# Optimization experiments

Measured on AMD Instinct MI355X. Metric: run time of the kernel, lower is better.

Reference implementation:

```python
import jax, jax.numpy as jnp
import numpy as np


def binarize_weight(w, scale=True):
    # Per-output-row mean-abs scale (dim=1 of [out, in]) times sign.
    # sign(0) -> 0 matches torch.sign semantics.
    s = jnp.mean(jnp.abs(w), axis=1, keepdims=True) if scale else jnp.ones((w.shape[0], 1), w.dtype)
    return jnp.sign(w) * s


def setup_inputs() -> dict:
    key = jax.random.key(0)
    kx, kw = jax.random.split(key)
    B, S, D_IN, D_OUT = 4, 2048, 4096, 4096
    x = jax.random.normal(kx, (B, S, D_IN), dtype=jnp.float32)
    # kaiming_normal_ with nonlinearity='linear': std = 1/sqrt(fan_in)
    weight = jax.random.normal(kw, (D_OUT, D_IN), dtype=jnp.float32) * (1.0 / np.sqrt(D_IN))
    return {"x": x, "weight": weight}


def reference(x, weight):
    w_b = binarize_weight(weight, scale=True)  # [out, in]
    # F.linear(x, w_b): x @ w_b.T
    return jnp.einsum("bsi,oi->bso", x, w_b)
```

## Files before the change

kernel.cpp:

```cpp
#include <hip/hip_runtime.h>
#include <hip/hip_bf16.h>
#include <stdint.h>

typedef int  iv4   __attribute__((ext_vector_type(4)));
typedef float f32x4 __attribute__((ext_vector_type(4)));

#define K_DIM 4096
#define N_DIM 4096

__global__ __launch_bounds__(256) void convert_x_i8(const float* __restrict__ x,
                                                    char* __restrict__ xq,
                                                    float* __restrict__ sx) {
    const int row = blockIdx.x;
    const int tid = threadIdx.x;
    const float* xr = x + (long long)row * K_DIM + tid * 16;

    float4 v0 = *(const float4*)(xr + 0);
    float4 v1 = *(const float4*)(xr + 4);
    float4 v2 = *(const float4*)(xr + 8);
    float4 v3 = *(const float4*)(xr + 12);

    float m = fabsf(v0.x);
    m = fmaxf(m, fabsf(v0.y)); m = fmaxf(m, fabsf(v0.z)); m = fmaxf(m, fabsf(v0.w));
    m = fmaxf(m, fabsf(v1.x)); m = fmaxf(m, fabsf(v1.y)); m = fmaxf(m, fabsf(v1.z)); m = fmaxf(m, fabsf(v1.w));
    m = fmaxf(m, fabsf(v2.x)); m = fmaxf(m, fabsf(v2.y)); m = fmaxf(m, fabsf(v2.z)); m = fmaxf(m, fabsf(v2.w));
    m = fmaxf(m, fabsf(v3.x)); m = fmaxf(m, fabsf(v3.y)); m = fmaxf(m, fabsf(v3.z)); m = fmaxf(m, fabsf(v3.w));

    #pragma unroll
    for (int d = 32; d > 0; d >>= 1) m = fmaxf(m, __shfl_xor(m, d));
    __shared__ float red[4];
    const int lane = tid & 63, wid = tid >> 6;
    if (lane == 0) red[wid] = m;
    __syncthreads();
    float rmax = fmaxf(fmaxf(red[0], red[1]), fmaxf(red[2], red[3]));
    rmax = fmaxf(rmax, 1e-20f);
    if (tid == 0) sx[row] = rmax * (1.0f / 127.0f);

    const float q = 127.0f / rmax;
    union { char c[16]; int4 v; } u;
    const float vals[16] = {v0.x, v0.y, v0.z, v0.w, v1.x, v1.y, v1.z, v1.w,
                            v2.x, v2.y, v2.z, v2.w, v3.x, v3.y, v3.z, v3.w};
    #pragma unroll
    for (int i = 0; i < 16; ++i) u.c[i] = (char)__float2int_rn(vals[i] * q);
    *(int4*)(xq + (long long)row * K_DIM + tid * 16) = u.v;
}

__global__ __launch_bounds__(256) void convert_w_i8(const float* __restrict__ w,
                                                    char* __restrict__ wq,
                                                    float* __restrict__ sw) {
    const int row = blockIdx.x;
    const int tid = threadIdx.x;
    const float* wr = w + (long long)row * K_DIM + tid * 16;

    float sum = 0.f;
    union { char c[16]; int4 v; } u;
    #pragma unroll
    for (int j = 0; j < 4; ++j) {
        float4 v = *(const float4*)(wr + j * 4);
        sum += fabsf(v.x) + fabsf(v.y) + fabsf(v.z) + fabsf(v.w);
        u.c[j * 4 + 0] = (char)((v.x > 0.f) - (v.x < 0.f));
        u.c[j * 4 + 1] = (char)((v.y > 0.f) - (v.y < 0.f));
        u.c[j * 4 + 2] = (char)((v.z > 0.f) - (v.z < 0.f));
        u.c[j * 4 + 3] = (char)((v.w > 0.f) - (v.w < 0.f));
    }
    *(int4*)(wq + (long long)row * K_DIM + tid * 16) = u.v;

    #pragma unroll
    for (int d = 32; d > 0; d >>= 1) sum += __shfl_down(sum, d);
    __shared__ float red[4];
    const int lane = tid & 63, wid = tid >> 6;
    if (lane == 0) red[wid] = sum;
    __syncthreads();
    if (tid == 0) sw[row] = (red[0] + red[1] + red[2] + red[3]) * (1.0f / (float)K_DIM);
}

struct SOp { const char* g; int row0; int kt; char* l; };

__device__ __forceinline__ void stage_half(const SOp s, int wid, int lane) {
    const int r      = s.row0 + wid * 16 + (lane >> 2);
    const int srcoff = s.kt + ((((lane & 3) ^ ((lane >> 3) & 3))) << 4);
    const char* src  = s.g + (long long)r * K_DIM + srcoff;
    __builtin_amdgcn_global_load_lds(
        (const __attribute__((address_space(1))) void*)src,
        (__attribute__((address_space(3))) void*)(s.l + wid * 1024), 16, 0, 0);
}

__device__ __forceinline__ iv4 ldsr(const char* t, int row, int c) {
    const int off = row * 64 + ((c ^ ((row >> 1) & 3)) << 4);
    return *(const iv4*)(t + off);
}

__device__ __forceinline__ void read_a0(iv4 (&a)[4], const char* tA, int wm, int l15, int c) {
    #pragma unroll
    for (int mi = 0; mi < 4; ++mi) a[mi] = ldsr(tA, wm * 128 + mi * 16 + l15, c);
}
__device__ __forceinline__ void read_a1(iv4 (&a)[4], const char* tA, int wm, int l15, int c) {
    #pragma unroll
    for (int mi = 0; mi < 4; ++mi) a[mi] = ldsr(tA, wm * 128 + 64 + mi * 16 + l15, c);
}
__device__ __forceinline__ void read_b0(iv4 (&b)[2], const char* tB, int wn, int l15, int c) {
    #pragma unroll
    for (int ni = 0; ni < 2; ++ni) b[ni] = ldsr(tB, wn * 64 + ni * 16 + l15, c);
}
__device__ __forceinline__ void read_b1(iv4 (&b)[2], const char* tB, int wn, int l15, int c) {
    #pragma unroll
    for (int ni = 0; ni < 2; ++ni) b[ni] = ldsr(tB, wn * 64 + 32 + ni * 16 + l15, c);
}

template<bool S0, bool S1, bool S2, bool S3, int WN>
__device__ __forceinline__ void kgroup(const char* __restrict__ tA,
                                       const char* __restrict__ tB,
                                       SOp s0, SOp s1, SOp s2, SOp s3,
                                       iv4 (&acc)[8][4],
                                       int wm, int wn, int wid, int lane)
{
    const int l15 = lane & 15;
    const int c   = lane >> 4;
    iv4 a0[4], a1[4], b0[2], b1[2];

    read_a0(a0, tA, wm, l15, c);
    read_b0(b0, tB, wn, l15, c);
    if constexpr (S0) stage_half(s0, wid, lane);
    __builtin_amdgcn_s_barrier();
    __builtin_amdgcn_s_setprio(1);
    #pragma unroll
    for (int mi = 0; mi < 4; ++mi)
        #pragma unroll
        for (int ni = 0; ni < 2; ++ni)
            acc[mi][ni] = __builtin_amdgcn_mfma_i32_16x16x64_i8(
                a0[mi], b0[ni], acc[mi][ni], 0, 0, 0);
    __builtin_amdgcn_s_setprio(0);
    __builtin_amdgcn_s_barrier();

    read_b1(b1, tB, wn, l15, c);
    if constexpr (S1) stage_half(s1, wid, lane);
    __builtin_amdgcn_s_barrier();
    __builtin_amdgcn_s_setprio(1);
    #pragma unroll
    for (int mi = 0; mi < 4; ++mi)
        #pragma unroll
        for (int ni = 0; ni < 2; ++ni)
            acc[mi][2 + ni] = __builtin_amdgcn_mfma_i32_16x16x64_i8(
                a0[mi], b1[ni], acc[mi][2 + ni], 0, 0, 0);
    __builtin_amdgcn_s_setprio(0);
    __builtin_amdgcn_s_barrier();

    read_a1(a1, tA, wm, l15, c);
    if constexpr (S2) stage_half(s2, wid, lane);
    __builtin_amdgcn_s_barrier();
    __builtin_amdgcn_s_setprio(1);
    #pragma unroll
    for (int mi = 0; mi < 4; ++mi)
        #pragma unroll
        for (int ni = 0; ni < 2; ++ni)
            acc[4 + mi][ni] = __builtin_amdgcn_mfma_i32_16x16x64_i8(
                a1[mi], b0[ni], acc[4 + mi][ni], 0, 0, 0);
    __builtin_amdgcn_s_setprio(0);
    __builtin_amdgcn_s_barrier();

    if constexpr (S3) stage_half(s3, wid, lane);
    __builtin_amdgcn_s_barrier();
    __builtin_amdgcn_s_setprio(1);
    #pragma unroll
    for (int mi = 0; mi < 4; ++mi)
        #pragma unroll
        for (int ni = 0; ni < 2; ++ni)
            acc[4 + mi][2 + ni] = __builtin_amdgcn_mfma_i32_16x16x64_i8(
                a1[mi], b1[ni], acc[4 + mi][2 + ni], 0, 0, 0);
    __builtin_amdgcn_s_setprio(0);
    if constexpr (WN == 1)      asm volatile("s_waitcnt vmcnt(1)" ::: "memory");
    else if constexpr (WN == 0) asm volatile("s_waitcnt vmcnt(0)" ::: "memory");
    if constexpr (WN >= 0) __builtin_amdgcn_s_barrier();
}

__global__ __launch_bounds__(512, 2) void bitlinear_gemm_i8(
    const char* __restrict__ A, const char* __restrict__ B,
    const float* __restrict__ sx, const float* __restrict__ sw,
    float* __restrict__ C, int M)
{
    extern __shared__ char smem[];
    char* As0 = smem;
    char* As1 = smem + 16384;
    char* Bs0 = smem + 32768;
    char* Bs1 = smem + 49152;

    const int tid = threadIdx.x, lane = tid & 63, wid = tid >> 6;
    const int wm = wid >> 2, wn = wid & 3;

    const int nbid = (int)blockIdx.x;
    const int cpx  = (int)gridDim.x >> 3;
    const int swz  = (nbid & 7) * cpx + (nbid >> 3);
    const int ntn  = N_DIM / 256;
    const int tm = swz / ntn, tn = swz % ntn;

    const char* gA = A + (long long)tm * 256 * K_DIM;
    const char* gB = B + (long long)tn * 256 * K_DIM;

    iv4 acc[8][4];
    #pragma unroll
    for (int i = 0; i < 8; ++i)
        #pragma unroll
        for (int j = 0; j < 4; ++j) acc[i][j] = (iv4){0, 0, 0, 0};

    stage_half({gA,   0,  0, As0},        wid, lane);
    stage_half({gA, 128,  0, As0 + 8192}, wid, lane);
    stage_half({gB,   0,  0, Bs0},        wid, lane);
    stage_half({gB, 128,  0, Bs0 + 8192}, wid, lane);
    stage_half({gA,   0, 64, As1},        wid, lane);
    asm volatile("s_waitcnt vmcnt(1)" ::: "memory");
    __builtin_amdgcn_s_barrier();

    kgroup<true, true, true, true, 1>(As0, Bs0,
        {gA, 128,  64, As1 + 8192}, {gB, 0,  64, Bs1},
        {gB, 128,  64, Bs1 + 8192}, {gA, 0, 128, As0},
        acc, wm, wn, wid, lane);
    #pragma unroll 1
    for (int i = 0; i < 30; ++i) {
        const int kt = (2 * i + 1) * 64;
        kgroup<true, true, true, true, 1>(As1, Bs1,
            {gA, 128, kt + 64,  As0 + 8192}, {gB, 0, kt + 64,  Bs0},
            {gB, 128, kt + 64,  Bs0 + 8192}, {gA, 0, kt + 128, As1},
            acc, wm, wn, wid, lane);
        kgroup<true, true, true, true, 1>(As0, Bs0,
            {gA, 128, kt + 128, As1 + 8192}, {gB, 0, kt + 128, Bs1},
            {gB, 128, kt + 128, Bs1 + 8192}, {gA, 0, kt + 192, As0},
            acc, wm, wn, wid, lane);
    }
    kgroup<true, true, true, true, 1>(As1, Bs1,
        {gA, 128, 62 * 64, As0 + 8192}, {gB, 0, 62 * 64, Bs0},
        {gB, 128, 62 * 64, Bs0 + 8192}, {gA, 0, 63 * 64, As1},
        acc, wm, wn, wid, lane);
    kgroup<true, true, true, false, 0>(As0, Bs0,
        {gA, 128, 63 * 64, As1 + 8192}, {gB, 0, 63 * 64, Bs1},
        {gB, 128, 63 * 64, Bs1 + 8192}, {gA, 0, 0, As0},
        acc, wm, wn, wid, lane);
    kgroup<false, false, false, false, -1>(As1, Bs1,
        {gA, 0, 0, As0}, {gA, 0, 0, As0}, {gA, 0, 0, As0}, {gA, 0, 0, As0},
        acc, wm, wn, wid, lane);

    const long long m0 = (long long)tm * 256 + wm * 128;
    const long long n0 = (long long)tn * 256 + wn * 64;
    float swv[4];
    #pragma unroll
    for (int ni = 0; ni < 4; ++ni) swv[ni] = sw[n0 + ni * 16 + (lane & 15)];
    #pragma unroll
    for (int mi = 0; mi < 8; ++mi) {
        const long long rowb = m0 + mi * 16 + (lane >> 4) * 4;
        float sxr[4];
        #pragma unroll
        for (int j = 0; j < 4; ++j) sxr[j] = sx[rowb + j];
        #pragma unroll
        for (int ni = 0; ni < 4; ++ni) {
            const long long col = n0 + ni * 16 + (lane & 15);
            #pragma unroll
            for (int j = 0; j < 4; ++j)
                C[(rowb + j) * N_DIM + col] = (float)acc[mi][ni][j] * swv[ni] * sxr[j];
        }
    }
}

__global__ void bitlinear_naive_kernel(const float* __restrict__ x,
                                       const float* __restrict__ w,
                                       float* __restrict__ out, long long total) {
    const long long idx = (long long)blockIdx.x * blockDim.x + threadIdx.x;
    if (idx >= total) return;
    const long long m = idx / N_DIM;
    const long long o = idx % N_DIM;
    const float* xr = x + m * K_DIM;
    const float* wrow = w + o * K_DIM;
    float sum = 0.f, sa = 0.f;
    for (int k = 0; k < K_DIM; ++k) {
        float wv = wrow[k];
        sa += fabsf(wv);
        sum += xr[k] * ((wv > 0.f) ? 1.f : ((wv < 0.f) ? -1.f : 0.f));
    }
    out[idx] = sum * (sa * (1.0f / (float)K_DIM));
}

extern "C" void kernel_launch(void* const* d_in, const int* in_sizes, int n_in,
                              void* d_out, int out_size, void* d_ws, size_t ws_size,
                              hipStream_t stream) {
    const float* x = (const float*)d_in[0];
    const float* w = (const float*)d_in[1];
    float* out = (float*)d_out;

    const int M = in_sizes[0] / K_DIM;

    const size_t xq_bytes = (size_t)M * K_DIM;
    const size_t wq_bytes = (size_t)N_DIM * K_DIM;
    const size_t sx_bytes = (size_t)M * sizeof(float);
    const size_t sw_bytes = (size_t)N_DIM * sizeof(float);

    if (ws_size < xq_bytes + wq_bytes + sx_bytes + sw_bytes || (M % 256) != 0) {
        const long long total = (long long)M * N_DIM;
        bitlinear_naive_kernel<<<(int)((total + 255) / 256), 256, 0, stream>>>(x, w, out, total);
        return;
    }

    char*  xq = (char*)d_ws;
    char*  wq = (char*)d_ws + xq_bytes;
    float* sx = (float*)((char*)d_ws + xq_bytes + wq_bytes);
    float* sw = (float*)((char*)d_ws + xq_bytes + wq_bytes + sx_bytes);

    convert_x_i8<<<M, 256, 0, stream>>>(x, xq, sx);
    convert_w_i8<<<N_DIM, 256, 0, stream>>>(w, wq, sw);

    hipFuncSetAttribute((const void*)bitlinear_gemm_i8,
                        hipFuncAttributeMaxDynamicSharedMemorySize, 65536);
    const int grid = (M / 256) * (N_DIM / 256);
    bitlinear_gemm_i8<<<grid, 512, 65536, stream>>>(xq, wq, sx, sw, out, M);
}
```

Measured before the change: 185.4 us.

## Triple-buffer LDS tiles and prefetch next tile's fragments into registers

Replaces the double-buffered LDS pipeline with a three-stage ring, so global loads for tile k+2 are issued while tile k is being computed. The A0/B0 register fragments for the next tile are read from LDS during the last MFMA phase of the current tile, overlapping LDS reads with compute. The wait is relaxed to vmcnt(3) so more loads stay in flight. Dynamic shared memory grows from 64KB to 96KB per block, which likely stops two 512-thread blocks from co-residing on a CU and lowers occupancy.

```diff
diff --git a/kernel.cpp b/kernel.cpp
--- a/kernel.cpp
+++ b/kernel.cpp
@@ -107,20 +107,24 @@
     for (int ni = 0; ni < 2; ++ni) b[ni] = ldsr(tB, wn * 64 + 32 + ni * 16 + l15, c);
 }
 
-template<bool S0, bool S1, bool S2, bool S3, int WN>
-__device__ __forceinline__ void kgroup(const char* __restrict__ tA,
-                                       const char* __restrict__ tB,
-                                       SOp s0, SOp s1, SOp s2, SOp s3,
-                                       iv4 (&acc)[8][4],
-                                       int wm, int wn, int wid, int lane)
+template<bool ST, int WN, bool RA>
+__device__ __forceinline__ void ktile(const char* __restrict__ cA,
+                                      const char* __restrict__ cB,
+                                      const char* __restrict__ oA,
+                                      const char* __restrict__ oB,
+                                      char* __restrict__ sA,
+                                      char* __restrict__ sB,
+                                      const char* gA, const char* gB, int kt2,
+                                      iv4 (&a0)[4], iv4 (&b0)[2],
+                                      iv4 (&acc)[8][4],
+                                      int wm, int wn, int wid, int lane)
 {
     const int l15 = lane & 15;
     const int c   = lane >> 4;
-    iv4 a0[4], a1[4], b0[2], b1[2];
-
-    read_a0(a0, tA, wm, l15, c);
-    read_b0(b0, tB, wn, l15, c);
-    if constexpr (S0) stage_half(s0, wid, lane);
+    iv4 a1[4], b1[2];
+
+    read_b1(b1, cB, wn, l15, c);
+    if constexpr (ST) stage_half({gA, 0, kt2, sA}, wid, lane);
     __builtin_amdgcn_s_barrier();
     __builtin_amdgcn_s_setprio(1);
     #pragma unroll
@@ -132,8 +136,8 @@
     __builtin_amdgcn_s_setprio(0);
     __builtin_amdgcn_s_barrier();
 
-    read_b1(b1, tB, wn, l15, c);
-    if constexpr (S1) stage_half(s1, wid, lane);
+    read_a1(a1, cA, wm, l15, c);
+    if constexpr (ST) stage_half({gA, 128, kt2, sA + 8192}, wid, lane);
     __builtin_amdgcn_s_barrier();
     __builtin_amdgcn_s_setprio(1);
     #pragma unroll
@@ -145,8 +149,7 @@
     __builtin_amdgcn_s_setprio(0);
     __builtin_amdgcn_s_barrier();
 
-    read_a1(a1, tA, wm, l15, c);
-    if constexpr (S2) stage_half(s2, wid, lane);
+    if constexpr (ST) stage_half({gB, 0, kt2, sB}, wid, lane);
     __builtin_amdgcn_s_barrier();
     __builtin_amdgcn_s_setprio(1);
     #pragma unroll
@@ -156,9 +159,16 @@
             acc[4 + mi][ni] = __builtin_amdgcn_mfma_i32_16x16x64_i8(
                 a1[mi], b0[ni], acc[4 + mi][ni], 0, 0, 0);
     __builtin_amdgcn_s_setprio(0);
-    __builtin_amdgcn_s_barrier();
-
-    if constexpr (S3) stage_half(s3, wid, lane);
+    if constexpr (WN == 3)      asm volatile("s_waitcnt vmcnt(3)" ::: "memory");
+    else if constexpr (WN == 0) asm volatile("s_waitcnt vmcnt(0)" ::: "memory");
+    __builtin_amdgcn_s_barrier();
+    if constexpr (RA) __builtin_amdgcn_sched_barrier(0);
+
+    if constexpr (RA) {
+        read_a0(a0, oA, wm, l15, c);
+        read_b0(b0, oB, wn, l15, c);
+    }
+    if constexpr (ST) stage_half({gB, 128, kt2, sB + 8192}, wid, lane);
     __builtin_amdgcn_s_barrier();
     __builtin_amdgcn_s_setprio(1);
     #pragma unroll
@@ -168,9 +178,7 @@
             acc[4 + mi][2 + ni] = __builtin_amdgcn_mfma_i32_16x16x64_i8(
                 a1[mi], b1[ni], acc[4 + mi][2 + ni], 0, 0, 0);
     __builtin_amdgcn_s_setprio(0);
-    if constexpr (WN == 1)      asm volatile("s_waitcnt vmcnt(1)" ::: "memory");
-    else if constexpr (WN == 0) asm volatile("s_waitcnt vmcnt(0)" ::: "memory");
-    if constexpr (WN >= 0) __builtin_amdgcn_s_barrier();
+    __builtin_amdgcn_s_barrier();
 }
 
 __global__ __launch_bounds__(512, 2) void bitlinear_gemm_i8(
@@ -181,11 +189,15 @@
     extern __shared__ char smem[];
     char* As0 = smem;
     char* As1 = smem + 16384;
-    char* Bs0 = smem + 32768;
-    char* Bs1 = smem + 49152;
+    char* As2 = smem + 32768;
+    char* Bs0 = smem + 49152;
+    char* Bs1 = smem + 65536;
+    char* Bs2 = smem + 81920;
 
     const int tid = threadIdx.x, lane = tid & 63, wid = tid >> 6;
     const int wm = wid >> 2, wn = wid & 3;
+    const int l15 = lane & 15;
+    const int c   = lane >> 4;
 
     const int nbid = (int)blockIdx.x;
     const int cpx  = (int)gridDim.x >> 3;
@@ -202,41 +214,40 @@
         #pragma unroll
         for (int j = 0; j < 4; ++j) acc[i][j] = (iv4){0, 0, 0, 0};
 
-    stage_half({gA,   0,  0, As0},        wid, lane);
-    stage_half({gA, 128,  0, As0 + 8192}, wid, lane);
-    stage_half({gB,   0,  0, Bs0},        wid, lane);
-    stage_half({gB, 128,  0, Bs0 + 8192}, wid, lane);
-    stage_half({gA,   0, 64, As1},        wid, lane);
-    asm volatile("s_waitcnt vmcnt(1)" ::: "memory");
-    __builtin_amdgcn_s_barrier();
-
-    kgroup<true, true, true, true, 1>(As0, Bs0,
-        {gA, 128,  64, As1 + 8192}, {gB, 0,  64, Bs1},
-        {gB, 128,  64, Bs1 + 8192}, {gA, 0, 128, As0},
-        acc, wm, wn, wid, lane);
+    stage_half({gA,   0,   0, As0},        wid, lane);
+    stage_half({gA, 128,   0, As0 + 8192}, wid, lane);
+    stage_half({gB,   0,   0, Bs0},        wid, lane);
+    stage_half({gB, 128,   0, Bs0 + 8192}, wid, lane);
+    stage_half({gA,   0,  64, As1},        wid, lane);
+    stage_half({gA, 128,  64, As1 + 8192}, wid, lane);
+    stage_half({gB,   0,  64, Bs1},        wid, lane);
+    stage_half({gB, 128,  64, Bs1 + 8192}, wid, lane);
+    asm volatile("s_waitcnt vmcnt(4)" ::: "memory");
+    __builtin_amdgcn_s_barrier();
+    __builtin_amdgcn_sched_barrier(0);
+
+    iv4 a0[4], b0[2];
+    read_a0(a0, As0, wm, l15, c);
+    read_b0(b0, Bs0, wn, l15, c);
+
     #pragma unroll 1
-    for (int i = 0; i < 30; ++i) {
-        const int kt = (2 * i + 1) * 64;
-        kgroup<true, true, true, true, 1>(As1, Bs1,
-            {gA, 128, kt + 64,  As0 + 8192}, {gB, 0, kt + 64,  Bs0},
-            {gB, 128, kt + 64,  Bs0 + 8192}, {gA, 0, kt + 128, As1},
-            acc, wm, wn, wid, lane);
-        kgroup<true, true, true, true, 1>(As0, Bs0,
-            {gA, 128, kt + 128, As1 + 8192}, {gB, 0, kt + 128, Bs1},
-            {gB, 128, kt + 128, Bs1 + 8192}, {gA, 0, kt + 192, As0},
-            acc, wm, wn, wid, lane);
-    }
-    kgroup<true, true, true, true, 1>(As1, Bs1,
-        {gA, 128, 62 * 64, As0 + 8192}, {gB, 0, 62 * 64, Bs0},
-        {gB, 128, 62 * 64, Bs0 + 8192}, {gA, 0, 63 * 64, As1},
-        acc, wm, wn, wid, lane);
-    kgroup<true, true, true, false, 0>(As0, Bs0,
-        {gA, 128, 63 * 64, As1 + 8192}, {gB, 0, 63 * 64, Bs1},
-        {gB, 128, 63 * 64, Bs1 + 8192}, {gA, 0, 0, As0},
-        acc, wm, wn, wid, lane);
-    kgroup<false, false, false, false, -1>(As1, Bs1,
-        {gA, 0, 0, As0}, {gA, 0, 0, As0}, {gA, 0, 0, As0}, {gA, 0, 0, As0},
-        acc, wm, wn, wid, lane);
+    for (int i = 0; i < 20; ++i) {
+        const int t = 3 * i;
+        ktile<true, 3, true>(As0, Bs0, As1, Bs1, As2, Bs2,
+                             gA, gB, (t + 2) * 64, a0, b0, acc, wm, wn, wid, lane);
+        ktile<true, 3, true>(As1, Bs1, As2, Bs2, As0, Bs0,
+                             gA, gB, (t + 3) * 64, a0, b0, acc, wm, wn, wid, lane);
+        ktile<true, 3, true>(As2, Bs2, As0, Bs0, As1, Bs1,
+                             gA, gB, (t + 4) * 64, a0, b0, acc, wm, wn, wid, lane);
+    }
+    ktile<true, 3, true>(As0, Bs0, As1, Bs1, As2, Bs2,
+                         gA, gB, 62 * 64, a0, b0, acc, wm, wn, wid, lane);
+    ktile<true, 3, true>(As1, Bs1, As2, Bs2, As0, Bs0,
+                         gA, gB, 63 * 64, a0, b0, acc, wm, wn, wid, lane);
+    ktile<false, 0, true>(As2, Bs2, As0, Bs0, As1, Bs1,
+                          gA, gB, 0, a0, b0, acc, wm, wn, wid, lane);
+    ktile<false, -1, false>(As0, Bs0, As1, Bs1, As2, Bs2,
+                            gA, gB, 0, a0, b0, acc, wm, wn, wid, lane);
 
     const long long m0 = (long long)tm * 256 + wm * 128;
     const long long n0 = (long long)tn * 256 + wn * 64;
@@ -306,7 +317,7 @@
     convert_w_i8<<<N_DIM, 256, 0, stream>>>(w, wq, sw);
 
     hipFuncSetAttribute((const void*)bitlinear_gemm_i8,
-                        hipFuncAttributeMaxDynamicSharedMemorySize, 65536);
+                        hipFuncAttributeMaxDynamicSharedMemorySize, 98304);
     const int grid = (M / 256) * (N_DIM / 256);
-    bitlinear_gemm_i8<<<grid, 512, 65536, stream>>>(xq, wq, sx, sw, out, M);
-}
+    bitlinear_gemm_i8<<<grid, 512, 98304, stream>>>(xq, wq, sx, sw, out, M);
+}
```

Measured after the change: 182.9 us. Within noise of the previous version (-1.3%).

## Replace interleaved barrier-phased k-group with barrier-free double-buffered k-tile loop

Applied to the files above, without the earlier changes.

Replaces the four-phase k-group, which interleaved global-to-LDS staging with MFMA phases under s_barrier and setprio, with a simpler per-tile step. Each step issues all staging for the next tile into the other buffer, reads all A/B fragments from the current buffer, runs 32 MFMAs back to back, then does one vmcnt(0) wait and one barrier. This cuts the number of barriers per k-tile and lets the compiler schedule freely. In exchange it gives up the fine-grained overlap and priority hints, and the full vmcnt(0) wait at the end of every tile can expose global-load latency.

```diff
diff --git a/kernel.cpp b/kernel.cpp
--- a/kernel.cpp
+++ b/kernel.cpp
@@ -107,70 +107,50 @@
     for (int ni = 0; ni < 2; ++ni) b[ni] = ldsr(tB, wn * 64 + 32 + ni * 16 + l15, c);
 }
 
-template<bool S0, bool S1, bool S2, bool S3, int WN>
-__device__ __forceinline__ void kgroup(const char* __restrict__ tA,
-                                       const char* __restrict__ tB,
-                                       SOp s0, SOp s1, SOp s2, SOp s3,
-                                       iv4 (&acc)[8][4],
-                                       int wm, int wn, int wid, int lane)
+template<bool ST, bool WB>
+__device__ __forceinline__ void ktile_free(const char* __restrict__ cA,
+                                           const char* __restrict__ cB,
+                                           char* __restrict__ sA,
+                                           char* __restrict__ sB,
+                                           const char* gA, const char* gB, int ktn,
+                                           iv4 (&acc)[8][4],
+                                           int wm, int wn, int wid, int lane)
 {
     const int l15 = lane & 15;
     const int c   = lane >> 4;
+
+    if constexpr (ST) {
+        stage_half({gA,   0, ktn, sA},        wid, lane);
+        stage_half({gA, 128, ktn, sA + 8192}, wid, lane);
+        stage_half({gB,   0, ktn, sB},        wid, lane);
+        stage_half({gB, 128, ktn, sB + 8192}, wid, lane);
+    }
+
     iv4 a0[4], a1[4], b0[2], b1[2];
-
-    read_a0(a0, tA, wm, l15, c);
-    read_b0(b0, tB, wn, l15, c);
-    if constexpr (S0) stage_half(s0, wid, lane);
-    __builtin_amdgcn_s_barrier();
-    __builtin_amdgcn_s_setprio(1);
-    #pragma unroll
-    for (int mi = 0; mi < 4; ++mi)
-        #pragma unroll
-        for (int ni = 0; ni < 2; ++ni)
+    read_a0(a0, cA, wm, l15, c);
+    read_b0(b0, cB, wn, l15, c);
+    read_b1(b1, cB, wn, l15, c);
+    read_a1(a1, cA, wm, l15, c);
+
+    #pragma unroll
+    for (int mi = 0; mi < 4; ++mi) {
+        #pragma unroll
+        for (int ni = 0; ni < 2; ++ni) {
             acc[mi][ni] = __builtin_amdgcn_mfma_i32_16x16x64_i8(
                 a0[mi], b0[ni], acc[mi][ni], 0, 0, 0);
-    __builtin_amdgcn_s_setprio(0);
-    __builtin_amdgcn_s_barrier();
-
-    read_b1(b1, tB, wn, l15, c);
-    if constexpr (S1) stage_half(s1, wid, lane);
-    __builtin_amdgcn_s_barrier();
-    __builtin_amdgcn_s_setprio(1);
-    #pragma unroll
-    for (int mi = 0; mi < 4; ++mi)
-        #pragma unroll
-        for (int ni = 0; ni < 2; ++ni)
             acc[mi][2 + ni] = __builtin_amdgcn_mfma_i32_16x16x64_i8(
                 a0[mi], b1[ni], acc[mi][2 + ni], 0, 0, 0);
-    __builtin_amdgcn_s_setprio(0);
-    __builtin_amdgcn_s_barrier();
-
-    read_a1(a1, tA, wm, l15, c);
-    if constexpr (S2) stage_half(s2, wid, lane);
-    __builtin_amdgcn_s_barrier();
-    __builtin_amdgcn_s_setprio(1);
-    #pragma unroll
-    for (int mi = 0; mi < 4; ++mi)
-        #pragma unroll
-        for (int ni = 0; ni < 2; ++ni)
             acc[4 + mi][ni] = __builtin_amdgcn_mfma_i32_16x16x64_i8(
                 a1[mi], b0[ni], acc[4 + mi][ni], 0, 0, 0);
-    __builtin_amdgcn_s_setprio(0);
-    __builtin_amdgcn_s_barrier();
-
-    if constexpr (S3) stage_half(s3, wid, lane);
-    __builtin_amdgcn_s_barrier();
-    __builtin_amdgcn_s_setprio(1);
-    #pragma unroll
-    for (int mi = 0; mi < 4; ++mi)
-        #pragma unroll
-        for (int ni = 0; ni < 2; ++ni)
             acc[4 + mi][2 + ni] = __builtin_amdgcn_mfma_i32_16x16x64_i8(
                 a1[mi], b1[ni], acc[4 + mi][2 + ni], 0, 0, 0);
-    __builtin_amdgcn_s_setprio(0);
-    if constexpr (WN == 1)      asm volatile("s_waitcnt vmcnt(1)" ::: "memory");
-    else if constexpr (WN == 0) asm volatile("s_waitcnt vmcnt(0)" ::: "memory");
-    if constexpr (WN >= 0) __builtin_amdgcn_s_barrier();
+        }
+    }
+
+    if constexpr (WB) {
+        asm volatile("s_waitcnt vmcnt(0)" ::: "memory");
+        __builtin_amdgcn_s_barrier();
+    }
 }
 
 __global__ __launch_bounds__(512, 2) void bitlinear_gemm_i8(
@@ -202,41 +182,24 @@
         #pragma unroll
         for (int j = 0; j < 4; ++j) acc[i][j] = (iv4){0, 0, 0, 0};
 
-    stage_half({gA,   0,  0, As0},        wid, lane);
-    stage_half({gA, 128,  0, As0 + 8192}, wid, lane);
-    stage_half({gB,   0,  0, Bs0},        wid, lane);
-    stage_half({gB, 128,  0, Bs0 + 8192}, wid, lane);
-    stage_half({gA,   0, 64, As1},        wid, lane);
-    asm volatile("s_waitcnt vmcnt(1)" ::: "memory");
+    stage_half({gA,   0, 0, As0},        wid, lane);
+    stage_half({gA, 128, 0, As0 + 8192}, wid, lane);
+    stage_half({gB,   0, 0, Bs0},        wid, lane);
+    stage_half({gB, 128, 0, Bs0 + 8192}, wid, lane);
+    asm volatile("s_waitcnt vmcnt(0)" ::: "memory");
     __builtin_amdgcn_s_barrier();
 
-    kgroup<true, true, true, true, 1>(As0, Bs0,
-        {gA, 128,  64, As1 + 8192}, {gB, 0,  64, Bs1},
-        {gB, 128,  64, Bs1 + 8192}, {gA, 0, 128, As0},
-        acc, wm, wn, wid, lane);
     #pragma unroll 1
-    for (int i = 0; i < 30; ++i) {
-        const int kt = (2 * i + 1) * 64;
-        kgroup<true, true, true, true, 1>(As1, Bs1,
-            {gA, 128, kt + 64,  As0 + 8192}, {gB, 0, kt + 64,  Bs0},
-            {gB, 128, kt + 64,  Bs0 + 8192}, {gA, 0, kt + 128, As1},
-            acc, wm, wn, wid, lane);
-        kgroup<true, true, true, true, 1>(As0, Bs0,
-            {gA, 128, kt + 128, As1 + 8192}, {gB, 0, kt + 128, Bs1},
-            {gB, 128, kt + 128, Bs1 + 8192}, {gA, 0, kt + 192, As0},
-            acc, wm, wn, wid, lane);
-    }
-    kgroup<true, true, true, true, 1>(As1, Bs1,
-        {gA, 128, 62 * 64, As0 + 8192}, {gB, 0, 62 * 64, Bs0},
-        {gB, 128, 62 * 64, Bs0 + 8192}, {gA, 0, 63 * 64, As1},
-        acc, wm, wn, wid, lane);
-    kgroup<true, true, true, false, 0>(As0, Bs0,
-        {gA, 128, 63 * 64, As1 + 8192}, {gB, 0, 63 * 64, Bs1},
-        {gB, 128, 63 * 64, Bs1 + 8192}, {gA, 0, 0, As0},
-        acc, wm, wn, wid, lane);
-    kgroup<false, false, false, false, -1>(As1, Bs1,
-        {gA, 0, 0, As0}, {gA, 0, 0, As0}, {gA, 0, 0, As0}, {gA, 0, 0, As0},
-        acc, wm, wn, wid, lane);
+    for (int i = 0; i < 31; ++i) {
+        ktile_free<true, true>(As0, Bs0, As1, Bs1, gA, gB, (2 * i + 1) * 64,
+                               acc, wm, wn, wid, lane);
+        ktile_free<true, true>(As1, Bs1, As0, Bs0, gA, gB, (2 * i + 2) * 64,
+                               acc, wm, wn, wid, lane);
+    }
+    ktile_free<true, true>(As0, Bs0, As1, Bs1, gA, gB, 63 * 64,
+                           acc, wm, wn, wid, lane);
+    ktile_free<false, false>(As1, Bs1, As0, Bs0, gA, gB, 0,
+                             acc, wm, wn, wid, lane);
 
     const long long m0 = (long long)tm * 256 + wm * 128;
     const long long n0 = (long long)tn * 256 + wn * 64;
```

Measured after the change: 198.3 us. 7.0% more time.

## Double GEMM K-tile depth to 128 bytes with 8-slot XOR LDS swizzle

Applied to the files above, without the earlier changes.

Doubles the int8 K-depth staged per pipeline step from 64 to 128 bytes. Each stage now issues two global-to-LDS loads per wave, uses a 128-byte row layout with an 8-way XOR swizzle, and runs two MFMA k-steps per quadrant. The goal is to halve the number of barrier-separated k-tiles and amortize synchronization and LDS read overhead over more MFMAs. The MFMA quadrant order is also rearranged into a snake so B fragments are reused. The cost is that LDS per block doubles to 128KB, which likely drops occupancy from two blocks to one per CU and reduces latency hiding.

```diff
diff --git a/kernel.cpp b/kernel.cpp
--- a/kernel.cpp
+++ b/kernel.cpp
@@ -7,6 +7,7 @@
 
 #define K_DIM 4096
 #define N_DIM 4096
+#define BKB   128
 
 __global__ __launch_bounds__(256) void convert_x_i8(const float* __restrict__ x,
                                                     char* __restrict__ xq,
@@ -77,98 +78,98 @@
 struct SOp { const char* g; int row0; int kt; char* l; };
 
 __device__ __forceinline__ void stage_half(const SOp s, int wid, int lane) {
-    const int r      = s.row0 + wid * 16 + (lane >> 2);
-    const int srcoff = s.kt + ((((lane & 3) ^ ((lane >> 3) & 3))) << 4);
-    const char* src  = s.g + (long long)r * K_DIM + srcoff;
-    __builtin_amdgcn_global_load_lds(
-        (const __attribute__((address_space(1))) void*)src,
-        (__attribute__((address_space(3))) void*)(s.l + wid * 1024), 16, 0, 0);
-}
-
-__device__ __forceinline__ iv4 ldsr(const char* t, int row, int c) {
-    const int off = row * 64 + ((c ^ ((row >> 1) & 3)) << 4);
-    return *(const iv4*)(t + off);
-}
-
-__device__ __forceinline__ void read_a0(iv4 (&a)[4], const char* tA, int wm, int l15, int c) {
-    #pragma unroll
-    for (int mi = 0; mi < 4; ++mi) a[mi] = ldsr(tA, wm * 128 + mi * 16 + l15, c);
-}
-__device__ __forceinline__ void read_a1(iv4 (&a)[4], const char* tA, int wm, int l15, int c) {
-    #pragma unroll
-    for (int mi = 0; mi < 4; ++mi) a[mi] = ldsr(tA, wm * 128 + 64 + mi * 16 + l15, c);
-}
-__device__ __forceinline__ void read_b0(iv4 (&b)[2], const char* tB, int wn, int l15, int c) {
-    #pragma unroll
-    for (int ni = 0; ni < 2; ++ni) b[ni] = ldsr(tB, wn * 64 + ni * 16 + l15, c);
-}
-__device__ __forceinline__ void read_b1(iv4 (&b)[2], const char* tB, int wn, int l15, int c) {
-    #pragma unroll
-    for (int ni = 0; ni < 2; ++ni) b[ni] = ldsr(tB, wn * 64 + 32 + ni * 16 + l15, c);
+    const int srcsw = ((lane & 7) ^ ((lane >> 3) & 7)) << 4;
+    #pragma unroll
+    for (int op = 0; op < 2; ++op) {
+        const int r = s.row0 + wid * 16 + op * 8 + (lane >> 3);
+        const char* src = s.g + (long long)r * K_DIM + s.kt + srcsw;
+        __builtin_amdgcn_global_load_lds(
+            (const __attribute__((address_space(1))) void*)src,
+            (__attribute__((address_space(3))) void*)(s.l + wid * 2048 + op * 1024),
+            16, 0, 0);
+    }
+}
+
+__device__ __forceinline__ iv4 ldsr(const char* t, int row, int slot) {
+    return *(const iv4*)(t + row * 128 + ((slot ^ (row & 7)) << 4));
+}
+
+__device__ __forceinline__ void read_ah(iv4 (&a)[4][2], const char* tA,
+                                        int wm, int h, int l15, int c) {
+    #pragma unroll
+    for (int mi = 0; mi < 4; ++mi)
+        #pragma unroll
+        for (int kk = 0; kk < 2; ++kk)
+            a[mi][kk] = ldsr(tA, wm * 128 + h * 64 + mi * 16 + l15, kk * 4 + c);
+}
+__device__ __forceinline__ void read_bv(iv4 (&b)[2][2], const char* tB,
+                                        int wn, int v, int l15, int c) {
+    #pragma unroll
+    for (int ni = 0; ni < 2; ++ni)
+        #pragma unroll
+        for (int kk = 0; kk < 2; ++kk)
+            b[ni][kk] = ldsr(tB, wn * 64 + v * 32 + ni * 16 + l15, kk * 4 + c);
+}
+
+template<int H, int V>
+__device__ __forceinline__ void mfma_q(iv4 (&acc)[8][4],
+                                       const iv4 (&a)[4][2], const iv4 (&b)[2][2]) {
+    #pragma unroll
+    for (int kk = 0; kk < 2; ++kk)
+        #pragma unroll
+        for (int mi = 0; mi < 4; ++mi)
+            #pragma unroll
+            for (int ni = 0; ni < 2; ++ni)
+                acc[H * 4 + mi][V * 2 + ni] = __builtin_amdgcn_mfma_i32_16x16x64_i8(
+                    a[mi][kk], b[ni][kk], acc[H * 4 + mi][V * 2 + ni], 0, 0, 0);
 }
 
 template<bool S0, bool S1, bool S2, bool S3, int WN>
-__device__ __forceinline__ void kgroup(const char* __restrict__ tA,
-                                       const char* __restrict__ tB,
-                                       SOp s0, SOp s1, SOp s2, SOp s3,
-                                       iv4 (&acc)[8][4],
-                                       int wm, int wn, int wid, int lane)
+__device__ __forceinline__ void ktile(const char* __restrict__ cA,
+                                      const char* __restrict__ cB,
+                                      char* __restrict__ oA,
+                                      char* __restrict__ oB,
+                                      char* __restrict__ curA,
+                                      const char* gA, const char* gB,
+                                      int ktn, int ktn2,
+                                      iv4 (&acc)[8][4],
+                                      int wm, int wn, int wid, int lane)
 {
     const int l15 = lane & 15;
     const int c   = lane >> 4;
-    iv4 a0[4], a1[4], b0[2], b1[2];
-
-    read_a0(a0, tA, wm, l15, c);
-    read_b0(b0, tB, wn, l15, c);
-    if constexpr (S0) stage_half(s0, wid, lane);
+    iv4 a[4][2], b0[2][2], b1[2][2];
+
+    read_ah(a, cA, wm, 0, l15, c);
+    read_bv(b0, cB, wn, 0, l15, c);
+    if constexpr (S0) stage_half({gA, 128, ktn, oA + 16384}, wid, lane);
     __builtin_amdgcn_s_barrier();
     __builtin_amdgcn_s_setprio(1);
-    #pragma unroll
-    for (int mi = 0; mi < 4; ++mi)
-        #pragma unroll
-        for (int ni = 0; ni < 2; ++ni)
-            acc[mi][ni] = __builtin_amdgcn_mfma_i32_16x16x64_i8(
-                a0[mi], b0[ni], acc[mi][ni], 0, 0, 0);
+    mfma_q<0, 0>(acc, a, b0);
     __builtin_amdgcn_s_setprio(0);
     __builtin_amdgcn_s_barrier();
 
-    read_b1(b1, tB, wn, l15, c);
-    if constexpr (S1) stage_half(s1, wid, lane);
+    read_bv(b1, cB, wn, 1, l15, c);
+    if constexpr (S1) stage_half({gB, 0, ktn, oB}, wid, lane);
     __builtin_amdgcn_s_barrier();
     __builtin_amdgcn_s_setprio(1);
-    #pragma unroll
-    for (int mi = 0; mi < 4; ++mi)
-        #pragma unroll
-        for (int ni = 0; ni < 2; ++ni)
-            acc[mi][2 + ni] = __builtin_amdgcn_mfma_i32_16x16x64_i8(
-                a0[mi], b1[ni], acc[mi][2 + ni], 0, 0, 0);
+    mfma_q<0, 1>(acc, a, b1);
     __builtin_amdgcn_s_setprio(0);
     __builtin_amdgcn_s_barrier();
 
-    read_a1(a1, tA, wm, l15, c);
-    if constexpr (S2) stage_half(s2, wid, lane);
+    read_ah(a, cA, wm, 1, l15, c);
+    if constexpr (S2) stage_half({gB, 128, ktn, oB + 16384}, wid, lane);
     __builtin_amdgcn_s_barrier();
     __builtin_amdgcn_s_setprio(1);
-    #pragma unroll
-    for (int mi = 0; mi < 4; ++mi)
-        #pragma unroll
-        for (int ni = 0; ni < 2; ++ni)
-            acc[4 + mi][ni] = __builtin_amdgcn_mfma_i32_16x16x64_i8(
-                a1[mi], b0[ni], acc[4 + mi][ni], 0, 0, 0);
+    mfma_q<1, 1>(acc, a, b1);
     __builtin_amdgcn_s_setprio(0);
     __builtin_amdgcn_s_barrier();
 
-    if constexpr (S3) stage_half(s3, wid, lane);
+    if constexpr (S3) stage_half({gA, 0, ktn2, curA}, wid, lane);
     __builtin_amdgcn_s_barrier();
     __builtin_amdgcn_s_setprio(1);
-    #pragma unroll
-    for (int mi = 0; mi < 4; ++mi)
-        #pragma unroll
-        for (int ni = 0; ni < 2; ++ni)
-            acc[4 + mi][2 + ni] = __builtin_amdgcn_mfma_i32_16x16x64_i8(
-                a1[mi], b1[ni], acc[4 + mi][2 + ni], 0, 0, 0);
+    mfma_q<1, 0>(acc, a, b0);
     __builtin_amdgcn_s_setprio(0);
-    if constexpr (WN == 1)      asm volatile("s_waitcnt vmcnt(1)" ::: "memory");
+    if constexpr (WN == 2)      asm volatile("s_waitcnt vmcnt(2)" ::: "memory");
     else if constexpr (WN == 0) asm volatile("s_waitcnt vmcnt(0)" ::: "memory");
     if constexpr (WN >= 0) __builtin_amdgcn_s_barrier();
 }
@@ -180,9 +181,9 @@
 {
     extern __shared__ char smem[];
     char* As0 = smem;
-    char* As1 = smem + 16384;
-    char* Bs0 = smem + 32768;
-    char* Bs1 = smem + 49152;
+    char* As1 = smem + 32768;
+    char* Bs0 = smem + 65536;
+    char* Bs1 = smem + 98304;
 
     const int tid = threadIdx.x, lane = tid & 63, wid = tid >> 6;
     const int wm = wid >> 2, wn = wid & 3;
@@ -202,41 +203,36 @@
         #pragma unroll
         for (int j = 0; j < 4; ++j) acc[i][j] = (iv4){0, 0, 0, 0};
 
-    stage_half({gA,   0,  0, As0},        wid, lane);
-    stage_half({gA, 128,  0, As0 + 8192}, wid, lane);
-    stage_half({gB,   0,  0, Bs0},        wid, lane);
-    stage_half({gB, 128,  0, Bs0 + 8192}, wid, lane);
-    stage_half({gA,   0, 64, As1},        wid, lane);
-    asm volatile("s_waitcnt vmcnt(1)" ::: "memory");
-    __builtin_amdgcn_s_barrier();
-
-    kgroup<true, true, true, true, 1>(As0, Bs0,
-        {gA, 128,  64, As1 + 8192}, {gB, 0,  64, Bs1},
-        {gB, 128,  64, Bs1 + 8192}, {gA, 0, 128, As0},
-        acc, wm, wn, wid, lane);
+    stage_half({gA,   0,   0, As0},         wid, lane);
+    stage_half({gA, 128,   0, As0 + 16384}, wid, lane);
+    stage_half({gB,   0,   0, Bs0},         wid, lane);
+    stage_half({gB, 128,   0, Bs0 + 16384}, wid, lane);
+    stage_half({gA,   0, BKB, As1},         wid, lane);
+    asm volatile("s_waitcnt vmcnt(2)" ::: "memory");
+    __builtin_amdgcn_s_barrier();
+
+    ktile<true, true, true, true, 2>(As0, Bs0, As1, Bs1, As0,
+                                     gA, gB, 1 * BKB, 2 * BKB,
+                                     acc, wm, wn, wid, lane);
     #pragma unroll 1
-    for (int i = 0; i < 30; ++i) {
-        const int kt = (2 * i + 1) * 64;
-        kgroup<true, true, true, true, 1>(As1, Bs1,
-            {gA, 128, kt + 64,  As0 + 8192}, {gB, 0, kt + 64,  Bs0},
-            {gB, 128, kt + 64,  Bs0 + 8192}, {gA, 0, kt + 128, As1},
-            acc, wm, wn, wid, lane);
-        kgroup<true, true, true, true, 1>(As0, Bs0,
-            {gA, 128, kt + 128, As1 + 8192}, {gB, 0, kt + 128, Bs1},
-            {gB, 128, kt + 128, Bs1 + 8192}, {gA, 0, kt + 192, As0},
-            acc, wm, wn, wid, lane);
-    }
-    kgroup<true, true, true, true, 1>(As1, Bs1,
-        {gA, 128, 62 * 64, As0 + 8192}, {gB, 0, 62 * 64, Bs0},
-        {gB, 128, 62 * 64, Bs0 + 8192}, {gA, 0, 63 * 64, As1},
-        acc, wm, wn, wid, lane);
-    kgroup<true, true, true, false, 0>(As0, Bs0,
-        {gA, 128, 63 * 64, As1 + 8192}, {gB, 0, 63 * 64, Bs1},
-        {gB, 128, 63 * 64, Bs1 + 8192}, {gA, 0, 0, As0},
-        acc, wm, wn, wid, lane);
-    kgroup<false, false, false, false, -1>(As1, Bs1,
-        {gA, 0, 0, As0}, {gA, 0, 0, As0}, {gA, 0, 0, As0}, {gA, 0, 0, As0},
-        acc, wm, wn, wid, lane);
+    for (int i = 0; i < 14; ++i) {
+        const int t = 2 * i + 1;
+        ktile<true, true, true, true, 2>(As1, Bs1, As0, Bs0, As1,
+                                         gA, gB, (t + 1) * BKB, (t + 2) * BKB,
+                                         acc, wm, wn, wid, lane);
+        ktile<true, true, true, true, 2>(As0, Bs0, As1, Bs1, As0,
+                                         gA, gB, (t + 2) * BKB, (t + 3) * BKB,
+                                         acc, wm, wn, wid, lane);
+    }
+    ktile<true, true, true, true, 2>(As1, Bs1, As0, Bs0, As1,
+                                     gA, gB, 30 * BKB, 31 * BKB,
+                                     acc, wm, wn, wid, lane);
+    ktile<true, true, true, false, 0>(As0, Bs0, As1, Bs1, As0,
+                                      gA, gB, 31 * BKB, 0,
+                                      acc, wm, wn, wid, lane);
+    ktile<false, false, false, false, -1>(As1, Bs1, As0, Bs0, As1,
+                                          gA, gB, 0, 0,
+                                          acc, wm, wn, wid, lane);
 
     const long long m0 = (long long)tm * 256 + wm * 128;
     const long long n0 = (long long)tn * 256 + wn * 64;
@@ -306,7 +302,7 @@
     convert_w_i8<<<N_DIM, 256, 0, stream>>>(w, wq, sw);
 
     hipFuncSetAttribute((const void*)bitlinear_gemm_i8,
-                        hipFuncAttributeMaxDynamicSharedMemorySize, 65536);
+                        hipFuncAttributeMaxDynamicSharedMemorySize, 131072);
     const int grid = (M / 256) * (N_DIM / 256);
-    bitlinear_gemm_i8<<<grid, 512, 65536, stream>>>(xq, wq, sx, sw, out, M);
-}
+    bitlinear_gemm_i8<<<grid, 512, 131072, stream>>>(xq, wq, sx, sw, out, M);
+}
```

Result: faster. 173.3 us (median of 3 runs) (-6.5%).
